# Performance work log

Hardware: AMD Instinct MI355X
Metric: run time of the kernel (lower is better)

Reference implementation:

```python
import jax, jax.numpy as jnp
import numpy as np

N = 40000      # nodes
E = 640000     # edges
G = 64         # graphs in batch
F_IN = 128
H = 128


def setup_inputs() -> dict:
    key = jax.random.key(0)
    ks = jax.random.split(key, 10)
    x = jax.random.normal(ks[0], (N, F_IN), dtype=jnp.float32)
    edge_index = jax.random.randint(ks[1], (2, E), 0, N, dtype=jnp.int64)
    batch = jnp.sort(jax.random.randint(ks[2], (N,), 0, G, dtype=jnp.int64))
    s = 0.05
    W1 = jax.random.normal(ks[3], (F_IN, H), dtype=jnp.float32) * s
    W2 = jax.random.normal(ks[4], (H, H), dtype=jnp.float32) * s
    W3 = jax.random.normal(ks[5], (H, H), dtype=jnp.float32) * s
    Wl = jax.random.normal(ks[6], (H, 1), dtype=jnp.float32) * s
    b1 = jnp.zeros((H,), jnp.float32)
    b2 = jnp.zeros((H,), jnp.float32)
    b3 = jnp.zeros((H,), jnp.float32)
    bl = jnp.zeros((1,), jnp.float32)
    return {"x": x, "edge_index": edge_index, "batch": batch, "dropout_rate": 0,
            "W1": W1, "b1": b1, "W2": W2, "b2": b2, "W3": W3, "b3": b3,
            "Wl": Wl, "bl": bl}


def _gcn_norm(edge_index, n):
    # PyG GCNConv default: add self-loops, symmetric deg^{-1/2} normalization.
    loop = jnp.arange(n, dtype=edge_index.dtype)
    row = jnp.concatenate([edge_index[0], loop])  # source
    col = jnp.concatenate([edge_index[1], loop])  # target
    ones = jnp.ones(row.shape[0], jnp.float32)
    deg = jax.ops.segment_sum(ones, col, num_segments=n)
    dis = jnp.where(deg > 0, jax.lax.rsqrt(deg), 0.0)
    norm = dis[row] * dis[col]  # [E+N]
    return row, col, norm


def _gcn_conv(x, row, col, norm, W, b, n):
    h = x @ W + b                       # dense transform [N,H]
    msg = h[row] * norm[:, None]        # gather + scale  [E+N,H]
    return jax.ops.segment_sum(msg, col, num_segments=n)


def reference(x, edge_index, batch, dropout_rate, W1, b1, W2, b2, W3, b3, Wl, bl):
    n = x.shape[0]
    row, col, norm = _gcn_norm(edge_index, n)
    # eval mode: dropout(p=dropout_rate, training=False) is identity
    h = jax.nn.relu(_gcn_conv(x, row, col, norm, W1, b1, n))
    h = jax.nn.relu(_gcn_conv(h, row, col, norm, W2, b2, n))
    h = jax.nn.relu(_gcn_conv(h, row, col, norm, W3, b3, n))
    # global mean pool over graphs
    sums = jax.ops.segment_sum(h, batch, num_segments=G)           # [G,H]
    cnt = jax.ops.segment_sum(jnp.ones(n, jnp.float32), batch, num_segments=G)
    pooled = sums / jnp.maximum(cnt, 1.0)[:, None]
    return pooled @ Wl + bl             # [G,1]
```

## Files before the change

kernel.cpp:

```cpp
#include <hip/hip_runtime.h>

constexpr int N = 40000;
constexpr int E = 640000;
constexpr int G = 64;
constexpr int H = 128;

constexpr int NB      = (N + 255) / 256;
constexpr int EB      = (E + 255) / 256;
constexpr int GEMM_B  = N / 32;
constexpr int FUSED_B = N / 32;
constexpr int CSR_MAX = E + 8 * N;

typedef float floatx2 __attribute__((ext_vector_type(2)));

__device__ __forceinline__ unsigned pack_fp8x4(float a, float b, float c, float d) {
    unsigned v = 0;
    v = __builtin_amdgcn_cvt_pk_fp8_f32(a, b, v, false);
    v = __builtin_amdgcn_cvt_pk_fp8_f32(c, d, v, true);
    return v;
}

__device__ __forceinline__ void fma8(float4& acc, unsigned r, int wbits) {
    float w = __int_as_float(wbits);
    floatx2 lo = __builtin_amdgcn_cvt_pk_f32_fp8(r, false);
    floatx2 hi = __builtin_amdgcn_cvt_pk_f32_fp8(r, true);
    acc.x = fmaf(lo.x, w, acc.x);
    acc.y = fmaf(lo.y, w, acc.y);
    acc.z = fmaf(hi.x, w, acc.z);
    acc.w = fmaf(hi.y, w, acc.w);
}

__device__ __forceinline__ float4 aggregate_node(const unsigned* __restrict__ h8,
                                                 const int4* __restrict__ csr4,
                                                 const int* __restrict__ row_ptr,
                                                 const float* __restrict__ dis,
                                                 int i, int c) {
    float d = dis[i];
    float sl = d * d;
    float4 acc = make_float4(0.f, 0.f, 0.f, 0.f);
    fma8(acc, h8[(size_t)i * 32 + c], __float_as_int(sl));
    int p  = row_ptr[i] >> 1;
    int p1 = row_ptr[i + 1] >> 1;
    for (; p < p1; p += 4) {
        int4 ea = csr4[p], eb = csr4[p + 1], ec = csr4[p + 2], ed = csr4[p + 3];
        unsigned r0 = h8[(size_t)ea.x * 32 + c], r1 = h8[(size_t)ea.z * 32 + c];
        unsigned r2 = h8[(size_t)eb.x * 32 + c], r3 = h8[(size_t)eb.z * 32 + c];
        unsigned r4 = h8[(size_t)ec.x * 32 + c], r5 = h8[(size_t)ec.z * 32 + c];
        unsigned r6 = h8[(size_t)ed.x * 32 + c], r7 = h8[(size_t)ed.z * 32 + c];
        fma8(acc, r0, ea.y); fma8(acc, r1, ea.w);
        fma8(acc, r2, eb.y); fma8(acc, r3, eb.w);
        fma8(acc, r4, ec.y); fma8(acc, r5, ec.w);
        fma8(acc, r6, ed.y); fma8(acc, r7, ed.w);
    }
    return acc;
}

__global__ __launch_bounds__(256) void gemm1_and_count(const float* __restrict__ X,
                                                       const float* __restrict__ W,
                                                       const float* __restrict__ b,
                                                       unsigned* __restrict__ Y,
                                                       const int* __restrict__ col,
                                                       int* __restrict__ deg) {
    __shared__ float4 Ws4[64 * 32];
    const int blk = blockIdx.x;
    const int tid = threadIdx.x;
    if (blk >= GEMM_B) {
        int e = (blk - GEMM_B) * 256 + tid;
        if (e < E) atomicAdd(&deg[col[e]], 1);
        return;
    }
    const int jg = tid & 31;
    const int rs = tid >> 5;
    const int r0 = blk * 32 + rs * 4;

    const float4* W4 = reinterpret_cast<const float4*>(W);
    const float4* X4 = reinterpret_cast<const float4*>(X);

    const float4 bv = reinterpret_cast<const float4*>(b)[jg];
    float4 acc0 = bv, acc1 = bv, acc2 = bv, acc3 = bv;

    for (int half = 0; half < 2; ++half) {
        #pragma unroll
        for (int i = 0; i < 8; ++i)
            Ws4[tid + i * 256] = W4[half * 2048 + tid + i * 256];
        __syncthreads();

        #pragma unroll 4
        for (int k4 = 0; k4 < 16; ++k4) {
            float4 xv0 = X4[(size_t)(r0 + 0) * 32 + half * 16 + k4];
            float4 xv1 = X4[(size_t)(r0 + 1) * 32 + half * 16 + k4];
            float4 xv2 = X4[(size_t)(r0 + 2) * 32 + half * 16 + k4];
            float4 xv3 = X4[(size_t)(r0 + 3) * 32 + half * 16 + k4];
            #pragma unroll
            for (int kk = 0; kk < 4; ++kk) {
                float4 wv = Ws4[(k4 * 4 + kk) * 32 + jg];
                float xs0 = (kk==0)?xv0.x:(kk==1)?xv0.y:(kk==2)?xv0.z:xv0.w;
                float xs1 = (kk==0)?xv1.x:(kk==1)?xv1.y:(kk==2)?xv1.z:xv1.w;
                float xs2 = (kk==0)?xv2.x:(kk==1)?xv2.y:(kk==2)?xv2.z:xv2.w;
                float xs3 = (kk==0)?xv3.x:(kk==1)?xv3.y:(kk==2)?xv3.z:xv3.w;
                acc0.x = fmaf(xs0, wv.x, acc0.x); acc0.y = fmaf(xs0, wv.y, acc0.y);
                acc0.z = fmaf(xs0, wv.z, acc0.z); acc0.w = fmaf(xs0, wv.w, acc0.w);
                acc1.x = fmaf(xs1, wv.x, acc1.x); acc1.y = fmaf(xs1, wv.y, acc1.y);
                acc1.z = fmaf(xs1, wv.z, acc1.z); acc1.w = fmaf(xs1, wv.w, acc1.w);
                acc2.x = fmaf(xs2, wv.x, acc2.x); acc2.y = fmaf(xs2, wv.y, acc2.y);
                acc2.z = fmaf(xs2, wv.z, acc2.z); acc2.w = fmaf(xs2, wv.w, acc2.w);
                acc3.x = fmaf(xs3, wv.x, acc3.x); acc3.y = fmaf(xs3, wv.y, acc3.y);
                acc3.z = fmaf(xs3, wv.z, acc3.z); acc3.w = fmaf(xs3, wv.w, acc3.w);
            }
        }
        __syncthreads();
    }

    Y[(size_t)(r0 + 0) * 32 + jg] = pack_fp8x4(acc0.x, acc0.y, acc0.z, acc0.w);
    Y[(size_t)(r0 + 1) * 32 + jg] = pack_fp8x4(acc1.x, acc1.y, acc1.z, acc1.w);
    Y[(size_t)(r0 + 2) * 32 + jg] = pack_fp8x4(acc2.x, acc2.y, acc2.z, acc2.w);
    Y[(size_t)(r0 + 3) * 32 + jg] = pack_fp8x4(acc3.x, acc3.y, acc3.z, acc3.w);
}

__global__ void dis_block_sum(const int* __restrict__ deg, float* __restrict__ dis,
                              int* __restrict__ part) {
    __shared__ int s[256];
    int i = blockIdx.x * 256 + threadIdx.x;
    int d = (i < N) ? deg[i] : 0;
    if (i < N) dis[i] = rsqrtf((float)(d + 1));
    s[threadIdx.x] = (d + 7) & ~7;
    __syncthreads();
    for (int off = 128; off > 0; off >>= 1) {
        if (threadIdx.x < off) s[threadIdx.x] += s[threadIdx.x + off];
        __syncthreads();
    }
    if (threadIdx.x == 0) part[blockIdx.x] = s[0];
}

__global__ void scan_write(const int* __restrict__ deg, const int* __restrict__ part,
                           int* __restrict__ row_ptr, int* __restrict__ cursor) {
    __shared__ int s[256];
    const int t = threadIdx.x;
    s[t] = (t < (int)blockIdx.x) ? part[t] : 0;
    __syncthreads();
    for (int o = 128; o > 0; o >>= 1) {
        if (t < o) s[t] += s[t + o];
        __syncthreads();
    }
    const int block_off = s[0];
    __syncthreads();
    int i = blockIdx.x * 256 + t;
    int val = (i < N) ? ((deg[i] + 7) & ~7) : 0;
    s[t] = val;
    __syncthreads();
    for (int o = 1; o < 256; o <<= 1) {
        int x = (t >= o) ? s[t - o] : 0;
        __syncthreads();
        s[t] += x;
        __syncthreads();
    }
    if (i < N) {
        int excl = s[t] - val + block_off;
        row_ptr[i] = excl;
        cursor[i] = excl;
        if (i == N - 1) row_ptr[N] = excl + val;
    }
}

__global__ void fill_csr(const int* __restrict__ row, const int* __restrict__ col,
                         const float* __restrict__ dis, int* __restrict__ cursor,
                         int2* __restrict__ csr) {
    int e = blockIdx.x * blockDim.x + threadIdx.x;
    if (e >= E) return;
    int r = row[e], c = col[e];
    float w = dis[r] * dis[c];
    int p = atomicAdd(&cursor[c], 1);
    csr[p] = make_int2(r, __float_as_int(w));
}

__global__ __launch_bounds__(256) void fused_agg_gemm(const unsigned* __restrict__ t_in,
                                                      const int4* __restrict__ csr4,
                                                      const int* __restrict__ row_ptr,
                                                      const float* __restrict__ dis,
                                                      const float* __restrict__ W,
                                                      const float* __restrict__ b,
                                                      unsigned* __restrict__ t_out) {
    __shared__ float4 tile[32 * 32];
    const int tid = threadIdx.x;
    const int node0 = blockIdx.x * 32;

    {
        const int c  = tid & 31;
        const int nl = tid >> 5;
        #pragma unroll
        for (int sub = 0; sub < 4; ++sub) {
            const int local = sub * 8 + nl;
            float4 acc = aggregate_node(t_in, csr4, row_ptr, dis, node0 + local, c);
            acc.x = fmaxf(acc.x, 0.f); acc.y = fmaxf(acc.y, 0.f);
            acc.z = fmaxf(acc.z, 0.f); acc.w = fmaxf(acc.w, 0.f);
            tile[local * 32 + c] = acc;
        }
    }
    __syncthreads();

    const int jg = tid & 31;
    const int rs = tid >> 5;
    const int r0 = rs * 4;
    const float4* W4 = reinterpret_cast<const float4*>(W);
    const float4 bv = reinterpret_cast<const float4*>(b)[jg];
    float4 acc0 = bv, acc1 = bv, acc2 = bv, acc3 = bv;

    #pragma unroll 4
    for (int k4 = 0; k4 < 32; ++k4) {
        float4 xv0 = tile[(r0 + 0) * 32 + k4];
        float4 xv1 = tile[(r0 + 1) * 32 + k4];
        float4 xv2 = tile[(r0 + 2) * 32 + k4];
        float4 xv3 = tile[(r0 + 3) * 32 + k4];
        #pragma unroll
        for (int kk = 0; kk < 4; ++kk) {
            float4 wv = W4[(k4 * 4 + kk) * 32 + jg];
            float xs0 = (kk==0)?xv0.x:(kk==1)?xv0.y:(kk==2)?xv0.z:xv0.w;
            float xs1 = (kk==0)?xv1.x:(kk==1)?xv1.y:(kk==2)?xv1.z:xv1.w;
            float xs2 = (kk==0)?xv2.x:(kk==1)?xv2.y:(kk==2)?xv2.z:xv2.w;
            float xs3 = (kk==0)?xv3.x:(kk==1)?xv3.y:(kk==2)?xv3.z:xv3.w;
            acc0.x = fmaf(xs0, wv.x, acc0.x); acc0.y = fmaf(xs0, wv.y, acc0.y);
            acc0.z = fmaf(xs0, wv.z, acc0.z); acc0.w = fmaf(xs0, wv.w, acc0.w);
            acc1.x = fmaf(xs1, wv.x, acc1.x); acc1.y = fmaf(xs1, wv.y, acc1.y);
            acc1.z = fmaf(xs1, wv.z, acc1.z); acc1.w = fmaf(xs1, wv.w, acc1.w);
            acc2.x = fmaf(xs2, wv.x, acc2.x); acc2.y = fmaf(xs2, wv.y, acc2.y);
            acc2.z = fmaf(xs2, wv.z, acc2.z); acc2.w = fmaf(xs2, wv.w, acc2.w);
            acc3.x = fmaf(xs3, wv.x, acc3.x); acc3.y = fmaf(xs3, wv.y, acc3.y);
            acc3.z = fmaf(xs3, wv.z, acc3.z); acc3.w = fmaf(xs3, wv.w, acc3.w);
        }
    }

    const int gr0 = node0 + r0;
    t_out[(size_t)(gr0 + 0) * 32 + jg] = pack_fp8x4(acc0.x, acc0.y, acc0.z, acc0.w);
    t_out[(size_t)(gr0 + 1) * 32 + jg] = pack_fp8x4(acc1.x, acc1.y, acc1.z, acc1.w);
    t_out[(size_t)(gr0 + 2) * 32 + jg] = pack_fp8x4(acc2.x, acc2.y, acc2.z, acc2.w);
    t_out[(size_t)(gr0 + 3) * 32 + jg] = pack_fp8x4(acc3.x, acc3.y, acc3.z, acc3.w);
}

__global__ __launch_bounds__(256) void agg_pool(const unsigned* __restrict__ t_in,
                                                const int4* __restrict__ csr4,
                                                const int* __restrict__ row_ptr,
                                                const float* __restrict__ dis,
                                                const int* __restrict__ batch,
                                                float* __restrict__ pooled) {
    __shared__ float4 tile[8 * 32];
    const int tid = threadIdx.x;
    const int c  = tid & 31;
    const int nl = tid >> 5;
    const int i0 = blockIdx.x * 8;

    float4 acc = aggregate_node(t_in, csr4, row_ptr, dis, i0 + nl, c);
    acc.x = fmaxf(acc.x, 0.f); acc.y = fmaxf(acc.y, 0.f);
    acc.z = fmaxf(acc.z, 0.f); acc.w = fmaxf(acc.w, 0.f);
    tile[nl * 32 + c] = acc;
    __syncthreads();

    if (tid < 128) {
        const int j = tid;
        const float* tf = reinterpret_cast<const float*>(tile);
        int cur = batch[i0];
        float s = 0.0f;
        #pragma unroll
        for (int r = 0; r < 8; ++r) {
            int g = batch[i0 + r];
            if (g != cur) { atomicAdd(&pooled[cur * H + j], s); s = 0.0f; cur = g; }
            s += tf[r * 128 + j];
        }
        atomicAdd(&pooled[cur * H + j], s);
    }
}

__global__ __launch_bounds__(128) void head(const float* __restrict__ pooled,
                                            const int* __restrict__ batch,
                                            const float* __restrict__ Wl,
                                            const float* __restrict__ bl,
                                            float* __restrict__ out) {
    const int g = blockIdx.x;
    const int j = threadIdx.x;
    __shared__ int bounds[2];
    if (j < 2) {
        int target = g + j;
        int lo = 0, hi = N;
        while (lo < hi) {
            int mid = (lo + hi) >> 1;
            if (batch[mid] < target) lo = mid + 1; else hi = mid;
        }
        bounds[j] = lo;
    }
    __syncthreads();
    float cnt = fmaxf((float)(bounds[1] - bounds[0]), 1.0f);
    float val = (pooled[g * H + j] / cnt) * Wl[j];
    __shared__ float red[128];
    red[j] = val;
    __syncthreads();
    #pragma unroll
    for (int s = 64; s > 0; s >>= 1) {
        if (j < s) red[j] += red[j + s];
        __syncthreads();
    }
    if (j == 0) out[g] = red[0] + bl[0];
}

extern "C" void kernel_launch(void* const* d_in, const int* in_sizes, int n_in,
                              void* d_out, int out_size, void* d_ws, size_t ws_size,
                              hipStream_t stream) {
    const float* x     = (const float*)d_in[0];
    const int*   ei    = (const int*)  d_in[1];
    const int*   batch = (const int*)  d_in[2];
    const float* W1 = (const float*)d_in[4];
    const float* b1 = (const float*)d_in[5];
    const float* W2 = (const float*)d_in[6];
    const float* b2 = (const float*)d_in[7];
    const float* W3 = (const float*)d_in[8];
    const float* b3 = (const float*)d_in[9];
    const float* Wl = (const float*)d_in[10];
    const float* bl = (const float*)d_in[11];
    float* out = (float*)d_out;

    const int* row = ei;
    const int* col = ei + E;

    auto align256 = [](size_t v) { return (v + 255) & ~(size_t)255; };
    char* ws = (char*)d_ws;
    size_t off = 0;
    int*   deg    = (int*)(ws + off);
    float* pooled = (float*)(deg + N);
    int2*  csr    = (int2*)(pooled + (size_t)G * H);
    size_t zero_bytes = (size_t)N * 4 + (size_t)G * H * 4 + (size_t)CSR_MAX * 8;
    off += align256(zero_bytes);
    float*    dis     = (float*)(ws + off); off += align256((size_t)N * 4);
    int*      row_ptr = (int*)  (ws + off); off += align256((size_t)(N + 1) * 4);
    int*      cursor  = (int*)  (ws + off); off += align256((size_t)N * 4);
    int*      part    = (int*)  (ws + off); off += align256((size_t)NB * 4);
    unsigned* bufA    = (unsigned*)(ws + off); off += align256((size_t)N * H);
    unsigned* bufB    = (unsigned*)(ws + off); off += align256((size_t)N * H);
    (void)ws_size; (void)n_in; (void)in_sizes; (void)out_size;

    const int4* csr4 = reinterpret_cast<const int4*>(csr);

    hipMemsetAsync(deg, 0, zero_bytes, stream);
    gemm1_and_count<<<GEMM_B + EB, 256, 0, stream>>>(x, W1, b1, bufA, col, deg);
    dis_block_sum<<<NB, 256, 0, stream>>>(deg, dis, part);
    scan_write<<<NB, 256, 0, stream>>>(deg, part, row_ptr, cursor);
    fill_csr<<<EB, 256, 0, stream>>>(row, col, dis, cursor, csr);
    fused_agg_gemm<<<FUSED_B, 256, 0, stream>>>(bufA, csr4, row_ptr, dis, W2, b2, bufB);
    fused_agg_gemm<<<FUSED_B, 256, 0, stream>>>(bufB, csr4, row_ptr, dis, W3, b3, bufA);
    agg_pool<<<N / 8, 256, 0, stream>>>(bufA, csr4, row_ptr, dis, batch, pooled);
    head<<<G, 128, 0, stream>>>(pooled, batch, Wl, bl, out);
}
```

Before: 266.5 us.

## Merge degree scan kernels into one and halve GEMM1 rows per block

After: 292.4 us. +9.7%, slower.

```diff
diff --git a/kernel.cpp b/kernel.cpp
--- a/kernel.cpp
+++ b/kernel.cpp
@@ -7,7 +7,7 @@
 
 constexpr int NB      = (N + 255) / 256;
 constexpr int EB      = (E + 255) / 256;
-constexpr int GEMM_B  = N / 32;
+constexpr int GEMM1_B = N / 16;
 constexpr int FUSED_B = N / 32;
 constexpr int CSR_MAX = E + 8 * N;
 
@@ -61,51 +61,43 @@
                                                        unsigned* __restrict__ Y,
                                                        const int* __restrict__ col,
                                                        int* __restrict__ deg) {
-    __shared__ float4 Ws4[64 * 32];
+    __shared__ float4 Ws4[32 * 32];
     const int blk = blockIdx.x;
     const int tid = threadIdx.x;
-    if (blk >= GEMM_B) {
-        int e = (blk - GEMM_B) * 256 + tid;
+    if (blk >= GEMM1_B) {
+        int e = (blk - GEMM1_B) * 256 + tid;
         if (e < E) atomicAdd(&deg[col[e]], 1);
         return;
     }
     const int jg = tid & 31;
     const int rs = tid >> 5;
-    const int r0 = blk * 32 + rs * 4;
+    const int r0 = blk * 16 + rs * 2;
 
     const float4* W4 = reinterpret_cast<const float4*>(W);
     const float4* X4 = reinterpret_cast<const float4*>(X);
 
     const float4 bv = reinterpret_cast<const float4*>(b)[jg];
-    float4 acc0 = bv, acc1 = bv, acc2 = bv, acc3 = bv;
-
-    for (int half = 0; half < 2; ++half) {
+    float4 acc0 = bv, acc1 = bv;
+
+    for (int q = 0; q < 4; ++q) {
         #pragma unroll
-        for (int i = 0; i < 8; ++i)
-            Ws4[tid + i * 256] = W4[half * 2048 + tid + i * 256];
+        for (int i = 0; i < 4; ++i)
+            Ws4[tid + i * 256] = W4[q * 1024 + tid + i * 256];
         __syncthreads();
 
         #pragma unroll 4
-        for (int k4 = 0; k4 < 16; ++k4) {
-            float4 xv0 = X4[(size_t)(r0 + 0) * 32 + half * 16 + k4];
-            float4 xv1 = X4[(size_t)(r0 + 1) * 32 + half * 16 + k4];
-            float4 xv2 = X4[(size_t)(r0 + 2) * 32 + half * 16 + k4];
-            float4 xv3 = X4[(size_t)(r0 + 3) * 32 + half * 16 + k4];
+        for (int k4 = 0; k4 < 8; ++k4) {
+            float4 xv0 = X4[(size_t)(r0 + 0) * 32 + q * 8 + k4];
+            float4 xv1 = X4[(size_t)(r0 + 1) * 32 + q * 8 + k4];
             #pragma unroll
             for (int kk = 0; kk < 4; ++kk) {
                 float4 wv = Ws4[(k4 * 4 + kk) * 32 + jg];
                 float xs0 = (kk==0)?xv0.x:(kk==1)?xv0.y:(kk==2)?xv0.z:xv0.w;
                 float xs1 = (kk==0)?xv1.x:(kk==1)?xv1.y:(kk==2)?xv1.z:xv1.w;
-                float xs2 = (kk==0)?xv2.x:(kk==1)?xv2.y:(kk==2)?xv2.z:xv2.w;
-                float xs3 = (kk==0)?xv3.x:(kk==1)?xv3.y:(kk==2)?xv3.z:xv3.w;
                 acc0.x = fmaf(xs0, wv.x, acc0.x); acc0.y = fmaf(xs0, wv.y, acc0.y);
                 acc0.z = fmaf(xs0, wv.z, acc0.z); acc0.w = fmaf(xs0, wv.w, acc0.w);
                 acc1.x = fmaf(xs1, wv.x, acc1.x); acc1.y = fmaf(xs1, wv.y, acc1.y);
                 acc1.z = fmaf(xs1, wv.z, acc1.z); acc1.w = fmaf(xs1, wv.w, acc1.w);
-                acc2.x = fmaf(xs2, wv.x, acc2.x); acc2.y = fmaf(xs2, wv.y, acc2.y);
-                acc2.z = fmaf(xs2, wv.z, acc2.z); acc2.w = fmaf(xs2, wv.w, acc2.w);
-                acc3.x = fmaf(xs3, wv.x, acc3.x); acc3.y = fmaf(xs3, wv.y, acc3.y);
-                acc3.z = fmaf(xs3, wv.z, acc3.z); acc3.w = fmaf(xs3, wv.w, acc3.w);
             }
         }
         __syncthreads();
@@ -113,39 +105,27 @@
 
     Y[(size_t)(r0 + 0) * 32 + jg] = pack_fp8x4(acc0.x, acc0.y, acc0.z, acc0.w);
     Y[(size_t)(r0 + 1) * 32 + jg] = pack_fp8x4(acc1.x, acc1.y, acc1.z, acc1.w);
-    Y[(size_t)(r0 + 2) * 32 + jg] = pack_fp8x4(acc2.x, acc2.y, acc2.z, acc2.w);
-    Y[(size_t)(r0 + 3) * 32 + jg] = pack_fp8x4(acc3.x, acc3.y, acc3.z, acc3.w);
-}
-
-__global__ void dis_block_sum(const int* __restrict__ deg, float* __restrict__ dis,
-                              int* __restrict__ part) {
+}
+
+__global__ void build_rowptr(const int* __restrict__ deg, float* __restrict__ dis,
+                             int* __restrict__ row_ptr, int* __restrict__ cursor) {
     __shared__ int s[256];
-    int i = blockIdx.x * 256 + threadIdx.x;
+    const int t = threadIdx.x;
+    const int base = blockIdx.x * 256;
+    int partial = 0;
+    for (int i = t; i < base; i += 256) partial += (deg[i] + 7) & ~7;
+    s[t] = partial;
+    __syncthreads();
+    for (int o = 128; o > 0; o >>= 1) {
+        if (t < o) s[t] += s[t + o];
+        __syncthreads();
+    }
+    const int block_off = s[0];
+    __syncthreads();
+    int i = base + t;
     int d = (i < N) ? deg[i] : 0;
     if (i < N) dis[i] = rsqrtf((float)(d + 1));
-    s[threadIdx.x] = (d + 7) & ~7;
-    __syncthreads();
-    for (int off = 128; off > 0; off >>= 1) {
-        if (threadIdx.x < off) s[threadIdx.x] += s[threadIdx.x + off];
-        __syncthreads();
-    }
-    if (threadIdx.x == 0) part[blockIdx.x] = s[0];
-}
-
-__global__ void scan_write(const int* __restrict__ deg, const int* __restrict__ part,
-                           int* __restrict__ row_ptr, int* __restrict__ cursor) {
-    __shared__ int s[256];
-    const int t = threadIdx.x;
-    s[t] = (t < (int)blockIdx.x) ? part[t] : 0;
-    __syncthreads();
-    for (int o = 128; o > 0; o >>= 1) {
-        if (t < o) s[t] += s[t + o];
-        __syncthreads();
-    }
-    const int block_off = s[0];
-    __syncthreads();
-    int i = blockIdx.x * 256 + t;
-    int val = (i < N) ? ((deg[i] + 7) & ~7) : 0;
+    int val = (i < N) ? ((d + 7) & ~7) : 0;
     s[t] = val;
     __syncthreads();
     for (int o = 1; o < 256; o <<= 1) {
@@ -330,7 +310,6 @@
     float*    dis     = (float*)(ws + off); off += align256((size_t)N * 4);
     int*      row_ptr = (int*)  (ws + off); off += align256((size_t)(N + 1) * 4);
     int*      cursor  = (int*)  (ws + off); off += align256((size_t)N * 4);
-    int*      part    = (int*)  (ws + off); off += align256((size_t)NB * 4);
     unsigned* bufA    = (unsigned*)(ws + off); off += align256((size_t)N * H);
     unsigned* bufB    = (unsigned*)(ws + off); off += align256((size_t)N * H);
     (void)ws_size; (void)n_in; (void)in_sizes; (void)out_size;
@@ -338,9 +317,8 @@
     const int4* csr4 = reinterpret_cast<const int4*>(csr);
 
     hipMemsetAsync(deg, 0, zero_bytes, stream);
-    gemm1_and_count<<<GEMM_B + EB, 256, 0, stream>>>(x, W1, b1, bufA, col, deg);
-    dis_block_sum<<<NB, 256, 0, stream>>>(deg, dis, part);
-    scan_write<<<NB, 256, 0, stream>>>(deg, part, row_ptr, cursor);
+    gemm1_and_count<<<GEMM1_B + EB, 256, 0, stream>>>(x, W1, b1, bufA, col, deg);
+    build_rowptr<<<NB, 256, 0, stream>>>(deg, dis, row_ptr, cursor);
     fill_csr<<<EB, 256, 0, stream>>>(row, col, dis, cursor, csr);
     fused_agg_gemm<<<FUSED_B, 256, 0, stream>>>(bufA, csr4, row_ptr, dis, W2, b2, bufB);
     fused_agg_gemm<<<FUSED_B, 256, 0, stream>>>(bufB, csr4, row_ptr, dis, W3, b3, bufA);
```

## Pack CSR entries into 32 bits with 24-bit source and fp8 weight

Applied to the files above, without the earlier changes.

Result: faster. 260.3 us (median of 2 runs) (-2.3%).

```diff
diff --git a/kernel.cpp b/kernel.cpp
--- a/kernel.cpp
+++ b/kernel.cpp
@@ -20,8 +20,7 @@
     return v;
 }
 
-__device__ __forceinline__ void fma8(float4& acc, unsigned r, int wbits) {
-    float w = __int_as_float(wbits);
+__device__ __forceinline__ void fma8(float4& acc, unsigned r, float w) {
     floatx2 lo = __builtin_amdgcn_cvt_pk_f32_fp8(r, false);
     floatx2 hi = __builtin_amdgcn_cvt_pk_f32_fp8(r, true);
     acc.x = fmaf(lo.x, w, acc.x);
@@ -29,6 +28,12 @@
     acc.z = fmaf(hi.x, w, acc.z);
     acc.w = fmaf(hi.y, w, acc.w);
 }
+
+__device__ __forceinline__ float entry_w(int e) {
+    floatx2 hi = __builtin_amdgcn_cvt_pk_f32_fp8((unsigned)e, true);
+    return hi.y;
+}
+__device__ __forceinline__ int entry_src(int e) { return e & 0xFFFFFF; }
 
 __device__ __forceinline__ float4 aggregate_node(const unsigned* __restrict__ h8,
                                                  const int4* __restrict__ csr4,
@@ -38,19 +43,23 @@
     float d = dis[i];
     float sl = d * d;
     float4 acc = make_float4(0.f, 0.f, 0.f, 0.f);
-    fma8(acc, h8[(size_t)i * 32 + c], __float_as_int(sl));
-    int p  = row_ptr[i] >> 1;
-    int p1 = row_ptr[i + 1] >> 1;
-    for (; p < p1; p += 4) {
-        int4 ea = csr4[p], eb = csr4[p + 1], ec = csr4[p + 2], ed = csr4[p + 3];
-        unsigned r0 = h8[(size_t)ea.x * 32 + c], r1 = h8[(size_t)ea.z * 32 + c];
-        unsigned r2 = h8[(size_t)eb.x * 32 + c], r3 = h8[(size_t)eb.z * 32 + c];
-        unsigned r4 = h8[(size_t)ec.x * 32 + c], r5 = h8[(size_t)ec.z * 32 + c];
-        unsigned r6 = h8[(size_t)ed.x * 32 + c], r7 = h8[(size_t)ed.z * 32 + c];
-        fma8(acc, r0, ea.y); fma8(acc, r1, ea.w);
-        fma8(acc, r2, eb.y); fma8(acc, r3, eb.w);
-        fma8(acc, r4, ec.y); fma8(acc, r5, ec.w);
-        fma8(acc, r6, ed.y); fma8(acc, r7, ed.w);
+    fma8(acc, h8[(size_t)i * 32 + c], sl);
+    int p  = row_ptr[i] >> 2;
+    int p1 = row_ptr[i + 1] >> 2;
+    for (; p < p1; p += 2) {
+        int4 ea = csr4[p], eb = csr4[p + 1];
+        unsigned r0 = h8[(size_t)entry_src(ea.x) * 32 + c];
+        unsigned r1 = h8[(size_t)entry_src(ea.y) * 32 + c];
+        unsigned r2 = h8[(size_t)entry_src(ea.z) * 32 + c];
+        unsigned r3 = h8[(size_t)entry_src(ea.w) * 32 + c];
+        unsigned r4 = h8[(size_t)entry_src(eb.x) * 32 + c];
+        unsigned r5 = h8[(size_t)entry_src(eb.y) * 32 + c];
+        unsigned r6 = h8[(size_t)entry_src(eb.z) * 32 + c];
+        unsigned r7 = h8[(size_t)entry_src(eb.w) * 32 + c];
+        fma8(acc, r0, entry_w(ea.x)); fma8(acc, r1, entry_w(ea.y));
+        fma8(acc, r2, entry_w(ea.z)); fma8(acc, r3, entry_w(ea.w));
+        fma8(acc, r4, entry_w(eb.x)); fma8(acc, r5, entry_w(eb.y));
+        fma8(acc, r6, entry_w(eb.z)); fma8(acc, r7, entry_w(eb.w));
     }
     return acc;
 }
@@ -164,13 +173,14 @@
 
 __global__ void fill_csr(const int* __restrict__ row, const int* __restrict__ col,
                          const float* __restrict__ dis, int* __restrict__ cursor,
-                         int2* __restrict__ csr) {
+                         int* __restrict__ csr) {
     int e = blockIdx.x * blockDim.x + threadIdx.x;
     if (e >= E) return;
     int r = row[e], c = col[e];
     float w = dis[r] * dis[c];
+    unsigned wb = __builtin_amdgcn_cvt_pk_fp8_f32(w, 0.0f, 0, false) & 0xFFu;
     int p = atomicAdd(&cursor[c], 1);
-    csr[p] = make_int2(r, __float_as_int(w));
+    csr[p] = (int)((wb << 24) | (unsigned)r);
 }
 
 __global__ __launch_bounds__(256) void fused_agg_gemm(const unsigned* __restrict__ t_in,
@@ -324,8 +334,8 @@
     size_t off = 0;
     int*   deg    = (int*)(ws + off);
     float* pooled = (float*)(deg + N);
-    int2*  csr    = (int2*)(pooled + (size_t)G * H);
-    size_t zero_bytes = (size_t)N * 4 + (size_t)G * H * 4 + (size_t)CSR_MAX * 8;
+    int*   csr    = (int*)(pooled + (size_t)G * H);
+    size_t zero_bytes = (size_t)N * 4 + (size_t)G * H * 4 + (size_t)CSR_MAX * 4;
     off += align256(zero_bytes);
     float*    dis     = (float*)(ws + off); off += align256((size_t)N * 4);
     int*      row_ptr = (int*)  (ws + off); off += align256((size_t)(N + 1) * 4);
```
